# Kernel tuning notes

Measured on AMD Instinct MI355X. Metric: run time of the kernel, lower is better.

The kernel has to match this reference:

```python
import jax, jax.numpy as jnp
import numpy as np

J = 17
SUBSETS = [[0, 5, 6, 11, 12], [7, 8, 13, 14], [9, 10, 15, 16]]


def _build_graph():
    # Physical (intra-level clique) and cross (adjacent-level bipartite) adjacency.
    phys = np.zeros((3, J, J), np.float32)
    cross = np.zeros((3, J, J), np.float32)
    for i, s in enumerate(SUBSETS):
        for u in s:
            for v in s:
                if u != v:
                    phys[i, u, v] = 1.0
        for off in (-1, 1):
            jl = i + off
            if 0 <= jl < 3:
                for u in s:
                    for v in SUBSETS[jl]:
                        cross[i, u, v] = 1.0
                        cross[i, v, u] = 1.0
    # Padded per-node neighbor lists for A_exp = phys + cross (static, tiny).
    nbr_idx, nbr_mask = [], []
    for i in range(3):
        A = phys[i] + cross[i]
        K = int((A > 0).sum(1).max())
        idx = np.zeros((J, K), np.int32)
        msk = np.zeros((J, K), bool)
        for jj in range(J):
            ns = np.nonzero(A[jj] > 0)[0]
            idx[jj, : len(ns)] = ns
            msk[jj, : len(ns)] = True
        nbr_idx.append(idx)
        nbr_mask.append(msk)
    return phys, nbr_idx, nbr_mask


PHYS, NBR_IDX, NBR_MASK = _build_graph()

N, HD, EH, OUT, IN = 8192, 64, 64, 128, 3


def setup_inputs() -> dict:
    key = jax.random.key(0)
    ks = jax.random.split(key, 12)

    def lin(kw, kb, o, i):
        s = 1.0 / np.sqrt(i)
        return (jax.random.uniform(kw, (o, i), minval=-s, maxval=s),
                jax.random.uniform(kb, (o,), minval=-s, maxval=s))

    inp = {
        "keypoints": jax.random.uniform(ks[0], (N, J, 2)) * 640.0,
        "scores": jax.random.uniform(ks[1], (N, J)),
    }
    inp["W0"], inp["b0"] = lin(ks[2], ks[3], HD, IN)
    inp["W1"], inp["b1"] = lin(ks[4], ks[5], HD, IN)
    inp["W2"], inp["b2"] = lin(ks[6], ks[7], HD, IN)
    inp["We"], inp["be"] = lin(ks[8], ks[9], EH, 2 * HD)
    inp["Wp"], inp["bp"] = lin(ks[10], ks[11], OUT, 3 * HD + 3 * EH)
    return inp


def _forward(keypoints, scores, W0, b0, W1, b1, W2, b2, We, be, Wp, bp):
    s = scores[..., None]                       # [N,J,1]
    mn = keypoints.min(axis=1, keepdims=True)   # per-detection min over joints
    mx = keypoints.max(axis=1, keepdims=True)
    k = (keypoints - mn) / (mx - mn + 1e-6)
    P = jnp.concatenate([k, s], axis=-1)        # [N,J,3]

    level_W = [(W0, b0), (W1, b1), (W2, b2)]
    pooled = []
    for i in range(3):
        W, b = level_W[i]
        h = jax.nn.relu(jnp.einsum('njd,hd->njh', P, W) + b)   # level MLP
        m = h * s
        H = jnp.einsum('uv,nvh->nuh', jnp.asarray(PHYS[i]), m)  # [N,J,HD]

        feat = H * s                                            # [N,J,HD]
        idx = jnp.asarray(NBR_IDX[i])                           # [J,K]
        mask = jnp.asarray(NBR_MASK[i], dtype=feat.dtype)       # [J,K]
        fj = feat[:, :, None, :]                                # [N,J,1,HD]
        fk = feat[:, idx, :]                                    # [N,J,K,HD]
        edge = jnp.concatenate([jnp.broadcast_to(fj, fk.shape), fk - fj], axis=-1)
        msgs = jax.nn.relu(jnp.einsum('njke,he->njkh', edge, We) + be)
        # msgs >= 0, so masking padded neighbors with 0 and taking max matches
        # torch's max over real neighbors, and yields 0 for neighbor-less joints.
        msgs = msgs * mask[None, :, :, None]
        Z = msgs.max(axis=2)                                    # [N,J,EH]
        pooled.append(jnp.concatenate([H, Z], axis=-1).mean(axis=1))

    final = jnp.concatenate(pooled, axis=-1)    # [N, 3*HD + 3*EH]
    return final @ Wp.T + bp                    # [N, OUT]


def reference(keypoints, scores, W0, b0, W1, b1, W2, b2, We, be, Wp, bp):
    return _forward(keypoints, scores, W0, b0, W1, b1, W2, b2, We, be, Wp, bp)
```

## Files before the change

kernel.cpp:

```cpp
#include <hip/hip_runtime.h>
#include <hip/hip_bf16.h>

#define DEVINL __device__ __forceinline__

using bf16 = __hip_bfloat16;
typedef __attribute__((ext_vector_type(8))) short short8v;
typedef __attribute__((ext_vector_type(4))) float float4v;

DEVINL unsigned short f2bu(float x) { return __bfloat16_as_ushort(__float2bfloat16(x)); }

DEVINL short8v pk8(float4 a, float4 b) {
    union { unsigned short u[8]; short8v v; } r;
    r.u[0] = f2bu(a.x); r.u[1] = f2bu(a.y); r.u[2] = f2bu(a.z); r.u[3] = f2bu(a.w);
    r.u[4] = f2bu(b.x); r.u[5] = f2bu(b.y); r.u[6] = f2bu(b.z); r.u[7] = f2bu(b.w);
    return r.v;
}

__global__ __launch_bounds__(256) void cvt_wp_kernel(
    const float* __restrict__ Wp, unsigned short* __restrict__ wpB) {
    int gid = blockIdx.x * 256 + threadIdx.x;
    float4 v = ((const float4*)Wp)[gid];
    union { unsigned short u[4]; uint2 d2; } pk;
    pk.u[0] = f2bu(v.x); pk.u[1] = f2bu(v.y);
    pk.u[2] = f2bu(v.z); pk.u[3] = f2bu(v.w);
    *(uint2*)&wpB[gid * 4] = pk.d2;
}


template <int BASE, int CNT, int OTH, int LVL>
DEVINL void do_lvl_mfma(const unsigned short (*featT)[16][72],
                        int lane, int t,
                        const short8v bA[2], const short8v bC[2],
                        float4v binit, unsigned short (*finS)[392]) {
    float4v zero = (float4v){0.f, 0.f, 0.f, 0.f};
    float4v aa[CNT], cc[CNT];
    int kq8 = (lane >> 4) * 8;
    int sl = lane & 15;
#pragma unroll
    for (int j = 0; j < CNT; ++j) {
        const unsigned short* base = &featT[BASE + j][sl][kq8];
        short8v a0 = *(const short8v*)base;
        short8v a1 = *(const short8v*)(base + 32);
        aa[j] = __builtin_amdgcn_mfma_f32_16x16x32_bf16(a0, bA[0], binit, 0, 0, 0);
        aa[j] = __builtin_amdgcn_mfma_f32_16x16x32_bf16(a1, bA[1], aa[j], 0, 0, 0);
        cc[j] = __builtin_amdgcn_mfma_f32_16x16x32_bf16(a0, bC[0], zero, 0, 0, 0);
        cc[j] = __builtin_amdgcn_mfma_f32_16x16x32_bf16(a1, bC[1], cc[j], 0, 0, 0);
    }
    float bet = binit[0];
#pragma unroll
    for (int r = 0; r < 4; ++r) {
        float a_[CNT], c_[CNT];
#pragma unroll
        for (int j = 0; j < CNT; ++j) { a_[j] = aa[j][r]; c_[j] = cc[j][r]; }
        float zs = 0.f;
#pragma unroll
        for (int j = 0; j < CNT; ++j) {
            float z = fmaxf(a_[j], 0.f);
#pragma unroll
            for (int k = 0; k < CNT; ++k) {
                if (k != j) z = fmaxf(z, a_[j] + c_[k]);
            }
            zs += z;
        }
        float zo = 0.f;
#pragma unroll
        for (int k = 0; k < CNT; ++k) zo = fmaxf(zo, bet + c_[k]);
        zs += (float)OTH * zo;
        int s = (lane >> 4) * 4 + r;
        finS[s][LVL * 128 + 64 + t] = f2bu(zs * (1.f / 17.f));
    }
}

__global__ __launch_bounds__(512) void hse_one_kernel(
    const float* __restrict__ kp, const float* __restrict__ sc,
    const float* __restrict__ W0, const float* __restrict__ b0,
    const float* __restrict__ W1, const float* __restrict__ b1,
    const float* __restrict__ W2, const float* __restrict__ b2,
    const float* __restrict__ We, const float* __restrict__ be,
    const unsigned short* __restrict__ wpB, const float* __restrict__ bp,
    float* __restrict__ out) {
    __shared__ float4 Praw[16][17];
    __shared__ unsigned short featT[13][16][72];
    __shared__ unsigned short finS[16][392];

    int tid = threadIdx.x;
    int w = tid >> 6;
    int lane = tid & 63;
    int sampBase = blockIdx.x * 16;

    int jj = lane & 31;
    int halfId = lane >> 5;
    int sMine = 2 * w + halfId;
    float xx = 0.f, yy = 0.f;
    if (jj < 17) {
        size_t base = (size_t)(sampBase + sMine) * 17 + jj;
        float2 xy = *(const float2*)(kp + base * 2);
        float ss = sc[base];
        xx = xy.x; yy = xy.y;
        Praw[sMine][jj] = make_float4(xx, yy, ss, 0.f);
    }

    int tile = w >> 1, parity = w & 1;
    int t2 = tile * 16 + (lane & 15);
    int kq8 = (lane >> 4) * 8;
    short8v bA[2], bC[2];
#pragma unroll
    for (int k = 0; k < 2; ++k) {
        int dbase = k * 32 + kq8;
        const float* r1 = We + t2 * 128 + dbase;
        const float* r2 = We + t2 * 128 + 64 + dbase;
        float4 x0 = *(const float4*)r1;
        float4 x1 = *(const float4*)(r1 + 4);
        float4 y0 = *(const float4*)r2;
        float4 y1 = *(const float4*)(r2 + 4);
        float4 d0 = make_float4(x0.x - y0.x, x0.y - y0.y, x0.z - y0.z, x0.w - y0.w);
        float4 d1 = make_float4(x1.x - y1.x, x1.y - y1.y, x1.z - y1.z, x1.w - y1.w);
        bA[k] = pk8(d0, d1);
        bC[k] = pk8(y0, y1);
    }
    float bet = be[t2];
    int o3 = w * 16 + (lane & 15);
    float bvout = bp[o3];

    float mnx = (jj < 17) ? xx : 1e30f, mxx = (jj < 17) ? xx : -1e30f;
    float mny = (jj < 17) ? yy : 1e30f, mxy = (jj < 17) ? yy : -1e30f;
#pragma unroll
    for (int off = 16; off; off >>= 1) {
        mnx = fminf(mnx, __shfl_xor(mnx, off, 32));
        mxx = fmaxf(mxx, __shfl_xor(mxx, off, 32));
        mny = fminf(mny, __shfl_xor(mny, off, 32));
        mxy = fmaxf(mxy, __shfl_xor(mxy, off, 32));
    }
    float ixl = 1.f / (mxx - mnx + 1e-6f);
    float iyl = 1.f / (mxy - mny + 1e-6f);
    float mnx_h[2], mny_h[2], ix_h[2], iy_h[2];
    mnx_h[0] = __shfl(mnx, 0);  mnx_h[1] = __shfl(mnx, 32);
    mny_h[0] = __shfl(mny, 0);  mny_h[1] = __shfl(mny, 32);
    ix_h[0] = __shfl(ixl, 0);   ix_h[1] = __shfl(ixl, 32);
    iy_h[0] = __shfl(iyl, 0);   iy_h[1] = __shfl(iyl, 32);

    {
        constexpr int JL[13]  = {0, 5, 6, 11, 12, 7, 8, 13, 14, 9, 10, 15, 16};
        constexpr int LEV[13] = {0, 0, 0, 0,  0,  1, 1, 1,  1,  2, 2,  2,  2};
        const float* Wls[3] = {W0, W1, W2};
        const float* bls[3] = {b0, b1, b2};
        float wx[3], wy[3], wsv[3], wb[3];
#pragma unroll
        for (int L = 0; L < 3; ++L) {
            wx[L] = Wls[L][lane * 3 + 0];
            wy[L] = Wls[L][lane * 3 + 1];
            wsv[L] = Wls[L][lane * 3 + 2];
            wb[L] = bls[L][lane];
        }

#pragma unroll
        for (int half = 0; half < 2; ++half) {
            int s = 2 * w + half;
            float mnxh = mnx_h[half], mnyh = mny_h[half];
            float ixh = ix_h[half], iyh = iy_h[half];

            float mj[13], sj[13];
            float msum[3] = {0.f, 0.f, 0.f};
#pragma unroll
            for (int q = 0; q < 13; ++q) {
                int j = JL[q];
                int L = LEV[q];
                float4 pv = Praw[s][j];
                float px = (pv.x - mnxh) * ixh;
                float py = (pv.y - mnyh) * iyh;
                float ps = pv.z;
                float h = fmaxf(px * wx[L] + py * wy[L] + ps * wsv[L] + wb[L], 0.f);
                float m = h * ps;
                mj[q] = m;
                sj[q] = ps;
                msum[L] += m;
            }
#pragma unroll
            for (int q = 0; q < 13; ++q) {
                featT[q][s][lane] = f2bu((msum[LEV[q]] - mj[q]) * sj[q]);
            }
            finS[s][0 * 128 + lane] = f2bu(4.f * msum[0] * (1.f / 17.f));
            finS[s][1 * 128 + lane] = f2bu(3.f * msum[1] * (1.f / 17.f));
            finS[s][2 * 128 + lane] = f2bu(3.f * msum[2] * (1.f / 17.f));
        }
    }
    __syncthreads();

    {
        float4v binit = (float4v){bet, bet, bet, bet};
        if (parity == 0) {
            do_lvl_mfma<0, 5, 4, 0>(featT, lane, t2, bA, bC, binit, finS);
        } else {
            do_lvl_mfma<5, 4, 9, 1>(featT, lane, t2, bA, bC, binit, finS);
            do_lvl_mfma<9, 4, 4, 2>(featT, lane, t2, bA, bC, binit, finS);
        }
    }
    __syncthreads();

    {
        const short8v* bptr = (const short8v*)(wpB + (size_t)o3 * 384 + kq8);
        float4v acc = (float4v){bvout, bvout, bvout, bvout};
#pragma unroll
        for (int kt = 0; kt < 12; ++kt) {
            short8v a = *(const short8v*)&finS[lane & 15][kt * 32 + kq8];
            short8v b = bptr[kt * 4];
            acc = __builtin_amdgcn_mfma_f32_16x16x32_bf16(a, b, acc, 0, 0, 0);
        }
        int srow = (lane >> 4) * 4;
#pragma unroll
        for (int r = 0; r < 4; ++r) {
            out[(size_t)(sampBase + srow + r) * 128 + o3] = acc[r];
        }
    }
}

template <int LI, int CNT, int OTH>
DEVINL void do_level_f(int w, int lane,
                       const float* __restrict__ Wl, const float* __restrict__ bl,
                       float mnx, float ix, float mny, float iy,
                       const float (*Praw)[17][3],
                       float (*featS)[64][8],
                       const float2 (*WW)[64],
                       const float* beS,
                       float (*finS)[384]) {
    constexpr int SUBJ[3][5] = {{0, 5, 6, 11, 12}, {7, 8, 13, 14, 16}, {9, 10, 15, 16, 16}};
    float w0 = Wl[lane * 3 + 0], w1 = Wl[lane * 3 + 1], w2 = Wl[lane * 3 + 2], bb = bl[lane];
    float mj[CNT], sj[CNT];
    float msum = 0.f;
#pragma unroll
    for (int jj = 0; jj < CNT; ++jj) {
        int j = SUBJ[LI][jj];
        float px = (Praw[w][j][0] - mnx) * ix;
        float py = (Praw[w][j][1] - mny) * iy;
        float ps = Praw[w][j][2];
        float h = fmaxf(px * w0 + py * w1 + ps * w2 + bb, 0.f);
        float m = h * ps;
        mj[jj] = m; sj[jj] = ps; msum += m;
    }
#pragma unroll
    for (int jj = 0; jj < CNT; ++jj) featS[w][lane][jj] = (msum - mj[jj]) * sj[jj];
    float Hsum = (float)(CNT - 1) * msum;
    __syncthreads();
    float a_[CNT], c_[CNT];
    float bet = beS[lane];
#pragma unroll
    for (int jj = 0; jj < CNT; ++jj) { a_[jj] = bet; c_[jj] = 0.f; }
#pragma unroll 4
    for (int d = 0; d < 64; ++d) {
        float2 wv = WW[d][lane];
        const float* fr = &featS[w][d][0];
        float4 f4 = *(const float4*)fr;
        float f[5];
        f[0] = f4.x; f[1] = f4.y; f[2] = f4.z; f[3] = f4.w; f[4] = 0.f;
        if constexpr (CNT > 4) f[4] = fr[4];
#pragma unroll
        for (int jj = 0; jj < CNT; ++jj) {
            a_[jj] = fmaf(wv.x, f[jj], a_[jj]);
            c_[jj] = fmaf(wv.y, f[jj], c_[jj]);
        }
    }
    __syncthreads();
    float zsum = 0.f;
#pragma unroll
    for (int jj = 0; jj < CNT; ++jj) {
        float z = fmaxf(a_[jj], 0.f);
#pragma unroll
        for (int kk = 0; kk < CNT; ++kk)
            if (kk != jj) z = fmaxf(z, a_[jj] + c_[kk]);
        zsum += z;
    }
    float zo = 0.f;
#pragma unroll
    for (int kk = 0; kk < CNT; ++kk) zo = fmaxf(zo, bet + c_[kk]);
    zsum += (float)OTH * zo;
    finS[w][LI * 128 + lane] = Hsum * (1.f / 17.f);
    finS[w][LI * 128 + 64 + lane] = zsum * (1.f / 17.f);
}

__global__ __launch_bounds__(256) void hse_fused_kernel(
    const float* __restrict__ kp, const float* __restrict__ sc,
    const float* __restrict__ W0, const float* __restrict__ b0,
    const float* __restrict__ W1, const float* __restrict__ b1,
    const float* __restrict__ W2, const float* __restrict__ b2,
    const float* __restrict__ We, const float* __restrict__ be,
    const float* __restrict__ Wp, const float* __restrict__ bp,
    float* __restrict__ out) {
    __shared__ float2 WW[64][64];
    __shared__ float beS[64];
    __shared__ float Praw[4][17][3];
    __shared__ float featS[4][64][8];
    __shared__ float finS[4][384];

    int tid = threadIdx.x;
    int w = tid >> 6;
    int lane = tid & 63;
    int sample = blockIdx.x * 4 + w;

    for (int i = tid; i < 4096; i += 256) {
        int t = i >> 6, d = i & 63;
        float wA = We[t * 128 + d];
        float wB = We[t * 128 + 64 + d];
        WW[d][t] = make_float2(wA - wB, wB);
    }
    if (tid < 64) beS[tid] = be[tid];
    if (lane < 17) {
        size_t base = (size_t)sample * 17 + lane;
        float2 xy = *(const float2*)(kp + base * 2);
        Praw[w][lane][0] = xy.x;
        Praw[w][lane][1] = xy.y;
        Praw[w][lane][2] = sc[base];
    }
    __syncthreads();

    float mnx = 1e30f, mxx = -1e30f, mny = 1e30f, mxy = -1e30f;
    for (int j = 0; j < 17; ++j) {
        float x = Praw[w][j][0], y = Praw[w][j][1];
        mnx = fminf(mnx, x); mxx = fmaxf(mxx, x);
        mny = fminf(mny, y); mxy = fmaxf(mxy, y);
    }
    float ix = 1.f / (mxx - mnx + 1e-6f);
    float iy = 1.f / (mxy - mny + 1e-6f);

    do_level_f<0, 5, 4>(w, lane, W0, b0, mnx, ix, mny, iy, Praw, featS, WW, beS, finS);
    do_level_f<1, 4, 9>(w, lane, W1, b1, mnx, ix, mny, iy, Praw, featS, WW, beS, finS);
    do_level_f<2, 4, 4>(w, lane, W2, b2, mnx, ix, mny, iy, Praw, featS, WW, beS, finS);
    __syncthreads();

    float acc0 = bp[lane];
    float acc1 = bp[64 + lane];
    const float* r0 = Wp + (size_t)lane * 384;
    const float* r1 = Wp + (size_t)(64 + lane) * 384;
    const float* fv = finS[w];
#pragma unroll 8
    for (int e = 0; e < 384; e += 4) {
        float4 wa = *(const float4*)(r0 + e);
        float4 wb = *(const float4*)(r1 + e);
        float4 ffv = *(const float4*)(fv + e);
        acc0 = fmaf(wa.x, ffv.x, acc0);
        acc0 = fmaf(wa.y, ffv.y, acc0);
        acc0 = fmaf(wa.z, ffv.z, acc0);
        acc0 = fmaf(wa.w, ffv.w, acc0);
        acc1 = fmaf(wb.x, ffv.x, acc1);
        acc1 = fmaf(wb.y, ffv.y, acc1);
        acc1 = fmaf(wb.z, ffv.z, acc1);
        acc1 = fmaf(wb.w, ffv.w, acc1);
    }
    out[(size_t)sample * 128 + lane] = acc0;
    out[(size_t)sample * 128 + 64 + lane] = acc1;
}

extern "C" void kernel_launch(void* const* d_in, const int* in_sizes, int n_in,
                              void* d_out, int out_size, void* d_ws, size_t ws_size,
                              hipStream_t stream) {
    const float* kp = (const float*)d_in[0];
    const float* sc = (const float*)d_in[1];
    const float* W0 = (const float*)d_in[2];
    const float* b0 = (const float*)d_in[3];
    const float* W1 = (const float*)d_in[4];
    const float* b1 = (const float*)d_in[5];
    const float* W2 = (const float*)d_in[6];
    const float* b2 = (const float*)d_in[7];
    const float* We = (const float*)d_in[8];
    const float* be = (const float*)d_in[9];
    const float* Wp = (const float*)d_in[10];
    const float* bp = (const float*)d_in[11];
    float* out = (float*)d_out;

    int N = in_sizes[0] / 34;
    size_t need = 49152 * sizeof(unsigned short);

    if (ws_size >= need) {
        unsigned short* wpB = (unsigned short*)d_ws;
        hipLaunchKernelGGL(cvt_wp_kernel, dim3(48), dim3(256), 0, stream, Wp, wpB);
        hipLaunchKernelGGL(hse_one_kernel, dim3(N / 16), dim3(512), 0, stream,
                           kp, sc, W0, b0, W1, b1, W2, b2, We, be, wpB, bp, out);
    } else {
        hipLaunchKernelGGL(hse_fused_kernel, dim3(N / 4), dim3(256), 0, stream,
                           kp, sc, W0, b0, W1, b1, W2, b2, We, be, Wp, bp, out);
    }
}
```

Measured before the change: 23.45 us.

## Remap edge MFMA so each warp handles its own samples, removing a block barrier

The edge-message MFMA stage is restructured so that each warp processes only the two samples it computed features for. Joints now sit on the MFMA row dimension, with featT transposed to [sample][joint][dim] and padded to 16 joints. Because no warp reads another warp's features, the __syncthreads between feature generation and the edge stage is dropped. In exchange each warp now loads and converts all four We tiles, pads rows to 16 (wasting some MFMA work), and redistributes results through many shuffles.

```diff
diff --git a/kernel.cpp b/kernel.cpp
--- a/kernel.cpp
+++ b/kernel.cpp
@@ -27,48 +27,22 @@
 }
 
 
-template <int BASE, int CNT, int OTH, int LVL>
-DEVINL void do_lvl_mfma(const unsigned short (*featT)[16][72],
-                        int lane, int t,
-                        const short8v bA[2], const short8v bC[2],
-                        float4v binit, unsigned short (*finS)[392]) {
-    float4v zero = (float4v){0.f, 0.f, 0.f, 0.f};
-    float4v aa[CNT], cc[CNT];
-    int kq8 = (lane >> 4) * 8;
-    int sl = lane & 15;
+template <int BASE, int CNT, int OTH>
+DEVINL float zsum_level(const float (&a_)[13], const float (&c_)[13], float bet) {
+    float zs = 0.f;
 #pragma unroll
     for (int j = 0; j < CNT; ++j) {
-        const unsigned short* base = &featT[BASE + j][sl][kq8];
-        short8v a0 = *(const short8v*)base;
-        short8v a1 = *(const short8v*)(base + 32);
-        aa[j] = __builtin_amdgcn_mfma_f32_16x16x32_bf16(a0, bA[0], binit, 0, 0, 0);
-        aa[j] = __builtin_amdgcn_mfma_f32_16x16x32_bf16(a1, bA[1], aa[j], 0, 0, 0);
-        cc[j] = __builtin_amdgcn_mfma_f32_16x16x32_bf16(a0, bC[0], zero, 0, 0, 0);
-        cc[j] = __builtin_amdgcn_mfma_f32_16x16x32_bf16(a1, bC[1], cc[j], 0, 0, 0);
-    }
-    float bet = binit[0];
-#pragma unroll
-    for (int r = 0; r < 4; ++r) {
-        float a_[CNT], c_[CNT];
-#pragma unroll
-        for (int j = 0; j < CNT; ++j) { a_[j] = aa[j][r]; c_[j] = cc[j][r]; }
-        float zs = 0.f;
-#pragma unroll
-        for (int j = 0; j < CNT; ++j) {
-            float z = fmaxf(a_[j], 0.f);
-#pragma unroll
-            for (int k = 0; k < CNT; ++k) {
-                if (k != j) z = fmaxf(z, a_[j] + c_[k]);
-            }
-            zs += z;
-        }
-        float zo = 0.f;
-#pragma unroll
-        for (int k = 0; k < CNT; ++k) zo = fmaxf(zo, bet + c_[k]);
-        zs += (float)OTH * zo;
-        int s = (lane >> 4) * 4 + r;
-        finS[s][LVL * 128 + 64 + t] = f2bu(zs * (1.f / 17.f));
-    }
+        float z = fmaxf(a_[BASE + j], 0.f);
+#pragma unroll
+        for (int k = 0; k < CNT; ++k) {
+            if (k != j) z = fmaxf(z, a_[BASE + j] + c_[BASE + k]);
+        }
+        zs += z;
+    }
+    float zo = 0.f;
+#pragma unroll
+    for (int k = 0; k < CNT; ++k) zo = fmaxf(zo, bet + c_[BASE + k]);
+    return zs + (float)OTH * zo;
 }
 
 __global__ __launch_bounds__(512) void hse_one_kernel(
@@ -80,7 +54,7 @@
     const unsigned short* __restrict__ wpB, const float* __restrict__ bp,
     float* __restrict__ out) {
     __shared__ float4 Praw[16][17];
-    __shared__ unsigned short featT[13][16][72];
+    __shared__ unsigned short featT[16][16][72];
     __shared__ unsigned short finS[16][392];
 
     int tid = threadIdx.x;
@@ -99,28 +73,6 @@
         xx = xy.x; yy = xy.y;
         Praw[sMine][jj] = make_float4(xx, yy, ss, 0.f);
     }
-
-    int tile = w >> 1, parity = w & 1;
-    int t2 = tile * 16 + (lane & 15);
-    int kq8 = (lane >> 4) * 8;
-    short8v bA[2], bC[2];
-#pragma unroll
-    for (int k = 0; k < 2; ++k) {
-        int dbase = k * 32 + kq8;
-        const float* r1 = We + t2 * 128 + dbase;
-        const float* r2 = We + t2 * 128 + 64 + dbase;
-        float4 x0 = *(const float4*)r1;
-        float4 x1 = *(const float4*)(r1 + 4);
-        float4 y0 = *(const float4*)r2;
-        float4 y1 = *(const float4*)(r2 + 4);
-        float4 d0 = make_float4(x0.x - y0.x, x0.y - y0.y, x0.z - y0.z, x0.w - y0.w);
-        float4 d1 = make_float4(x1.x - y1.x, x1.y - y1.y, x1.z - y1.z, x1.w - y1.w);
-        bA[k] = pk8(d0, d1);
-        bC[k] = pk8(y0, y1);
-    }
-    float bet = be[t2];
-    int o3 = w * 16 + (lane & 15);
-    float bvout = bp[o3];
 
     float mnx = (jj < 17) ? xx : 1e30f, mxx = (jj < 17) ? xx : -1e30f;
     float mny = (jj < 17) ? yy : 1e30f, mxy = (jj < 17) ? yy : -1e30f;
@@ -177,28 +129,80 @@
             }
 #pragma unroll
             for (int q = 0; q < 13; ++q) {
-                featT[q][s][lane] = f2bu((msum[LEV[q]] - mj[q]) * sj[q]);
+                featT[s][q][lane] = f2bu((msum[LEV[q]] - mj[q]) * sj[q]);
             }
             finS[s][0 * 128 + lane] = f2bu(4.f * msum[0] * (1.f / 17.f));
             finS[s][1 * 128 + lane] = f2bu(3.f * msum[1] * (1.f / 17.f));
             finS[s][2 * 128 + lane] = f2bu(3.f * msum[2] * (1.f / 17.f));
         }
     }
-    __syncthreads();
 
     {
-        float4v binit = (float4v){bet, bet, bet, bet};
-        if (parity == 0) {
-            do_lvl_mfma<0, 5, 4, 0>(featT, lane, t2, bA, bC, binit, finS);
-        } else {
-            do_lvl_mfma<5, 4, 9, 1>(featT, lane, t2, bA, bC, binit, finS);
-            do_lvl_mfma<9, 4, 4, 2>(featT, lane, t2, bA, bC, binit, finS);
+        int t = lane & 15;
+        int kq8 = (lane >> 4) * 8;
+        float4v zero = (float4v){0.f, 0.f, 0.f, 0.f};
+#pragma unroll
+        for (int tile = 0; tile < 4; ++tile) {
+            int tt = tile * 16 + t;
+            short8v bA[2], bC[2];
+#pragma unroll
+            for (int k = 0; k < 2; ++k) {
+                int dbase = k * 32 + kq8;
+                const float* r1 = We + tt * 128 + dbase;
+                const float* r2 = We + tt * 128 + 64 + dbase;
+                float4 x0 = *(const float4*)r1;
+                float4 x1 = *(const float4*)(r1 + 4);
+                float4 y0 = *(const float4*)r2;
+                float4 y1 = *(const float4*)(r2 + 4);
+                float4 d0 = make_float4(x0.x - y0.x, x0.y - y0.y, x0.z - y0.z, x0.w - y0.w);
+                float4 d1 = make_float4(x1.x - y1.x, x1.y - y1.y, x1.z - y1.z, x1.w - y1.w);
+                bA[k] = pk8(d0, d1);
+                bC[k] = pk8(y0, y1);
+            }
+            float bet = be[tt];
+            float4v binit = (float4v){bet, bet, bet, bet};
+
+#pragma unroll
+            for (int half = 0; half < 2; ++half) {
+                int s = 2 * w + half;
+                const unsigned short* abase = &featT[s][lane & 15][kq8];
+                short8v a0 = *(const short8v*)abase;
+                short8v a1 = *(const short8v*)(abase + 32);
+                float4v aa = __builtin_amdgcn_mfma_f32_16x16x32_bf16(a0, bA[0], binit, 0, 0, 0);
+                aa = __builtin_amdgcn_mfma_f32_16x16x32_bf16(a1, bA[1], aa, 0, 0, 0);
+                float4v cc = __builtin_amdgcn_mfma_f32_16x16x32_bf16(a0, bC[0], zero, 0, 0, 0);
+                cc = __builtin_amdgcn_mfma_f32_16x16x32_bf16(a1, bC[1], cc, 0, 0, 0);
+
+                float a_[13], c_[13];
+#pragma unroll
+                for (int Q = 0; Q < 3; ++Q) {
+#pragma unroll
+                    for (int r = 0; r < 4; ++r) {
+                        a_[Q * 4 + r] = __shfl(aa[r], Q * 16 + t);
+                        c_[Q * 4 + r] = __shfl(cc[r], Q * 16 + t);
+                    }
+                }
+                a_[12] = __shfl(aa[0], 48 + t);
+                c_[12] = __shfl(cc[0], 48 + t);
+
+                float z0 = zsum_level<0, 5, 4>(a_, c_, bet);
+                float z1 = zsum_level<5, 4, 9>(a_, c_, bet);
+                float z2 = zsum_level<9, 4, 4>(a_, c_, bet);
+                if (lane < 16) {
+                    finS[s][0 * 128 + 64 + tt] = f2bu(z0 * (1.f / 17.f));
+                    finS[s][1 * 128 + 64 + tt] = f2bu(z1 * (1.f / 17.f));
+                    finS[s][2 * 128 + 64 + tt] = f2bu(z2 * (1.f / 17.f));
+                }
+            }
         }
     }
     __syncthreads();
 
     {
+        int o3 = w * 16 + (lane & 15);
+        int kq8 = (lane >> 4) * 8;
         const short8v* bptr = (const short8v*)(wpB + (size_t)o3 * 384 + kq8);
+        float bvout = bp[o3];
         float4v acc = (float4v){bvout, bvout, bvout, bvout};
 #pragma unroll
         for (int kt = 0; kt < 12; ++kt) {
```

After: 35.38 us. 1.51x slower.
